# Kernel optimization log

Measured on AMD Instinct MI355X. Metric: run time of the kernel, lower is better.

Reference implementation:

```python
import jax, jax.numpy as jnp
import numpy as np
from jax import lax

NUM_L2 = 9
# hierarchical validity table: level1 pred 0 -> classes 0..3, pred 1 -> classes 4..8
_VALID = np.full((2, NUM_L2), -np.inf, dtype=np.float32)
_VALID[0, 0:4] = 0.0
_VALID[1, 4:9] = 0.0
MASK_TABLE = jnp.asarray(_VALID)


def setup_inputs() -> dict:
    key = jax.random.key(0)
    ks = jax.random.split(key, 8)
    B, C, H, W = 64, 18, 224, 224
    x = jax.random.normal(ks[0], (B, C, H, W), dtype=jnp.float32)
    model1_pred = jax.random.normal(ks[1], (B, 2), dtype=jnp.float32)
    conv_w = jax.random.normal(ks[2], (32, 18, 3, 3), dtype=jnp.float32) * 0.05
    conv_b = jax.random.normal(ks[3], (32,), dtype=jnp.float32) * 0.05
    fc1_w = jax.random.normal(ks[4], (64, 34), dtype=jnp.float32) * 0.05
    fc1_b = jax.random.normal(ks[5], (64,), dtype=jnp.float32) * 0.05
    fc2_w = jax.random.normal(ks[6], (NUM_L2, 64), dtype=jnp.float32) * 0.05
    fc2_b = jax.random.normal(ks[7], (NUM_L2,), dtype=jnp.float32) * 0.05
    return {"x": x, "model1_pred": model1_pred, "conv_w": conv_w, "conv_b": conv_b,
            "fc1_w": fc1_w, "fc1_b": fc1_b, "fc2_w": fc2_w, "fc2_b": fc2_b}


def reference(x, model1_pred, conv_w, conv_b, fc1_w, fc1_b, fc2_w, fc2_b):
    # conv 18->32, k3, pad 1 (SAME), NCHW
    h = lax.conv_general_dilated(
        x, conv_w, window_strides=(1, 1), padding='SAME',
        dimension_numbers=('NCHW', 'OIHW', 'NCHW'))
    h = jax.nn.relu(h + conv_b[None, :, None, None])
    g = h.mean(axis=(2, 3))                          # [B, 32] global average pool
    f = jnp.concatenate([g, model1_pred], axis=1)    # [B, 34]
    f = jax.nn.relu(f @ fc1_w.T + fc1_b)             # [B, 64]
    logits = f @ fc2_w.T + fc2_b                     # [B, 9]
    idx = jnp.argmax(model1_pred, axis=1)            # [B] level-1 prediction
    mask = MASK_TABLE[idx]                           # gather instead of host loop
    return jax.nn.softmax(logits + mask, axis=1)
```

## Files before the change

kernel.cpp:

```cpp
#include <hip/hip_runtime.h>
#include <math.h>

typedef _Float16 f16;
typedef _Float16 f16x2 __attribute__((ext_vector_type(2)));
typedef _Float16 f16x8 __attribute__((ext_vector_type(8)));
typedef float f32x16 __attribute__((ext_vector_type(16)));

#define BATCH 64
#define IC 18
#define OC 32
#define H 224
#define W 224
#define RSTRIP 28
#define NSTRIP 8
#define NTILE 7
#define WPB 4
#define KPW (NTILE * NSTRIP)
#define UNITS (BATCH * KPW)
#define NBLOCK (UNITS / WPB)
#define RECS 34
#define RECW 24
#define SLOTF (RECS * RECW)
#define BSTRIDE 72
#define NUM_L2 9

#define MF(a_, b_, c_) c_ = __builtin_amdgcn_mfma_f32_32x32x16_f16((a_), (b_), (c_), 0, 0, 0)

__global__ __launch_bounds__(256, 4)
void conv_mfma_kernel(const float* __restrict__ x,
                      const float* __restrict__ conv_w,
                      const float* __restrict__ conv_b,
                      float* __restrict__ part) {
    __shared__ __align__(16) f16 slab[WPB][4][SLOTF];
    __shared__ __align__(16) f16 Bw[3 * 32 * BSTRIDE];

    const int tid = threadIdx.x;
    const int l   = tid & 63;
    const int wv  = tid >> 6;
    const int lm  = l & 31;
    const int lh  = l >> 5;

    const int unit = blockIdx.x * WPB + wv;
    const int b    = unit / KPW;
    const int rem  = unit - b * KPW;
    const int t    = rem % NTILE;
    const int s    = rem / NTILE;
    const int r0   = s * RSTRIP;
    const int col0 = t * 32 - 1;

    for (int idx = tid; idx < 3 * 32 * 64; idx += 256) {
        const int kh = idx >> 11;
        const int oc = (idx >> 6) & 31;
        const int kp = idx & 63;
        int kw = 0, ic = 0, valid = 1;
        if (kp < 18)      { kw = 0; ic = kp; }
        else if (kp < 20) { kw = 2; ic = 16 + (kp - 18); }
        else if (kp < 24) { valid = 0; }
        else if (kp < 42) { kw = 1; ic = kp - 24; }
        else if (kp < 48) { valid = 0; }
        else              { kw = 2; ic = kp - 48; }
        Bw[(kh * 32 + oc) * BSTRIDE + kp] =
            (f16)(valid ? conv_w[oc * 162 + ic * 9 + kh * 3 + kw] : 0.f);
    }

    for (int i = l; i < 4 * RECS; i += 64) {
        const int sl  = i / RECS;
        const int rec = i - sl * RECS;
        f16* q = &slab[wv][sl][rec * RECW];
        f16x2 z2; z2[0] = (f16)0.f; z2[1] = (f16)0.f;
        *reinterpret_cast<f16x2*>(&q[20]) = z2;
        *reinterpret_cast<f16x2*>(&q[22]) = z2;
        if (rec >= 32) *reinterpret_cast<f16x2*>(&q[18]) = z2;
    }
    __syncthreads();

    const int p   = l >> 1;
    const int hh  = l & 1;
    const int col = col0 + p;
    const bool colok = (col >= 0) & (col < W);
    const size_t plane = (size_t)H * W;
    const float* xb = x + ((size_t)b * IC + 8 * hh) * plane + col;
    const int er   = 32 + (l >> 1);
    const int ecol = col0 + er;
    const bool eok = (l < 4) & (ecol < W);
    const float* xe = x + ((size_t)b * IC + 8 * hh) * plane + ecol;

    auto STAGE_LOAD = [&](int g, float* sv, float* sve) {
        const bool rok = (g >= 0) & (g < H);
        if (rok & colok) {
            const float* q = xb + (size_t)g * W;
            #pragma unroll
            for (int j = 0; j < 8; ++j) sv[j] = q[j * plane];
            if (hh) { sv[8] = q[8 * plane]; sv[9] = q[9 * plane]; }
            else    { sv[8] = 0.f; sv[9] = 0.f; }
        } else {
            #pragma unroll
            for (int j = 0; j < 10; ++j) sv[j] = 0.f;
        }
        if (l < 4) {
            if (rok & eok) {
                const float* q = xe + (size_t)g * W;
                #pragma unroll
                for (int j = 0; j < 8; ++j) sve[j] = q[j * plane];
                if (hh) { sve[8] = q[8 * plane]; sve[9] = q[9 * plane]; }
                else    { sve[8] = 0.f; sve[9] = 0.f; }
            } else {
                #pragma unroll
                for (int j = 0; j < 10; ++j) sve[j] = 0.f;
            }
        }
    };
    auto STAGE_WRITE = [&](int slot, const float* sv, const float* sve) {
        f16* sw = &slab[wv][slot][0];
        f16x8 v;
        #pragma unroll
        for (int j = 0; j < 8; ++j) v[j] = (f16)sv[j];
        *reinterpret_cast<f16x8*>(&sw[p * RECW + 8 * hh]) = v;
        if (hh) {
            f16x2 c2; c2[0] = (f16)sv[8]; c2[1] = (f16)sv[9];
            *reinterpret_cast<f16x2*>(&sw[p * RECW + 16]) = c2;
            if (p >= 2)
                *reinterpret_cast<f16x2*>(&sw[(p - 2) * RECW + 18]) = c2;
        }
        if (l < 4) {
            f16x8 w8;
            #pragma unroll
            for (int j = 0; j < 8; ++j) w8[j] = (f16)sve[j];
            *reinterpret_cast<f16x8*>(&sw[er * RECW + 8 * hh]) = w8;
            if (hh) {
                f16x2 e2; e2[0] = (f16)sve[8]; e2[1] = (f16)sve[9];
                *reinterpret_cast<f16x2*>(&sw[er * RECW + 16]) = e2;
                *reinterpret_cast<f16x2*>(&sw[(er - 2) * RECW + 18]) = e2;
            }
        }
    };

    for (int g = r0 - 1; g <= r0 + 1; ++g) {
        float sv[10], sve[10];
        STAGE_LOAD(g, sv, sve);
        STAGE_WRITE(g & 3, sv, sve);
    }

    f16x8 bfr[3][4];
    #pragma unroll
    for (int kh = 0; kh < 3; ++kh)
        #pragma unroll
        for (int cc = 0; cc < 4; ++cc)
            bfr[kh][cc] = *reinterpret_cast<const f16x8*>(
                &Bw[(kh * 32 + lm) * BSTRIDE + 16 * cc + 8 * lh]);

    const float bias = conv_b[lm];
    float pacc = 0.f;
    f32x16 acc;
    #pragma unroll
    for (int i = 0; i < 16; ++i) acc[i] = 0.f;

    const int abase = RECW * lm + 8 * lh;

    for (int r = r0; r < r0 + RSTRIP; ++r) {
        const bool do_stage = (r != r0 + RSTRIP - 1);
        float sv[10], sve[10];
        if (do_stage) STAGE_LOAD(r + 2, sv, sve);

        #pragma unroll
        for (int kh = 0; kh < 3; ++kh) {
            const f16* sb = &slab[wv][(r - 1 + kh) & 3][0];
            const f16x8 a0 = *reinterpret_cast<const f16x8*>(&sb[abase]);
            const f16x8 a1 = *reinterpret_cast<const f16x8*>(&sb[abase + 16]);
            const f16x8 a2 = *reinterpret_cast<const f16x8*>(&sb[abase + 32]);
            const f16x8 a3 = *reinterpret_cast<const f16x8*>(&sb[abase + 48]);
            MF(a0, bfr[kh][0], acc); MF(a1, bfr[kh][1], acc);
            MF(a2, bfr[kh][2], acc); MF(a3, bfr[kh][3], acc);
        }

        float ssum = 0.f;
        #pragma unroll
        for (int i = 0; i < 16; ++i) ssum += fmaxf(acc[i] + bias, 0.f);
        pacc += ssum;
        #pragma unroll
        for (int i = 0; i < 16; ++i) acc[i] = 0.f;

        if (do_stage) STAGE_WRITE((r + 2) & 3, sv, sve);
    }

    pacc += __shfl_xor(pacc, 32);
    if (l < 32) part[((size_t)b * KPW + rem) * 32 + lm] = pacc;
}

__global__ void head_kernel(const float* __restrict__ part,
                            const float* __restrict__ pred,
                            const float* __restrict__ fc1_w,
                            const float* __restrict__ fc1_b,
                            const float* __restrict__ fc2_w,
                            const float* __restrict__ fc2_b,
                            float* __restrict__ out) {
    __shared__ float feat[34];
    __shared__ float fsh[64];
    __shared__ float lsh[NUM_L2];
    const int b = blockIdx.x;
    const int tI = threadIdx.x;

    if (tI < 32) {
        float sres = 0.f;
        const float* pp = part + (size_t)b * KPW * 32 + tI;
        for (int k = 0; k < KPW; ++k) sres += pp[k * 32];
        feat[tI] = sres * (1.f / (float)(H * W));
    } else if (tI < 34) {
        feat[tI] = pred[b * 2 + (tI - 32)];
    }
    __syncthreads();

    {
        float sum = fc1_b[tI];
        #pragma unroll
        for (int k = 0; k < 34; ++k) sum += feat[k] * fc1_w[tI * 34 + k];
        fsh[tI] = fmaxf(sum, 0.f);
    }
    __syncthreads();

    if (tI < NUM_L2) {
        float sum = fc2_b[tI];
        #pragma unroll
        for (int j = 0; j < 64; ++j) sum += fsh[j] * fc2_w[tI * 64 + j];
        lsh[tI] = sum;
    }
    __syncthreads();

    if (tI == 0) {
        const int idx = (pred[b * 2 + 1] > pred[b * 2 + 0]) ? 1 : 0;
        const int lo = idx ? 4 : 0;
        const int hi = idx ? 9 : 4;
        float m = -1e30f;
        for (int c = lo; c < hi; ++c) m = fmaxf(m, lsh[c]);
        float e[NUM_L2];
        float ssum = 0.f;
        for (int c = 0; c < NUM_L2; ++c) {
            const float v = (c >= lo && c < hi) ? expf(lsh[c] - m) : 0.f;
            e[c] = v;
            ssum += v;
        }
        const float rs = 1.f / ssum;
        for (int c = 0; c < NUM_L2; ++c) out[b * NUM_L2 + c] = e[c] * rs;
    }
}

extern "C" void kernel_launch(void* const* d_in, const int* in_sizes, int n_in,
                              void* d_out, int out_size, void* d_ws, size_t ws_size,
                              hipStream_t stream) {
    const float* x      = (const float*)d_in[0];
    const float* pred   = (const float*)d_in[1];
    const float* conv_w = (const float*)d_in[2];
    const float* conv_b = (const float*)d_in[3];
    const float* fc1_w  = (const float*)d_in[4];
    const float* fc1_b  = (const float*)d_in[5];
    const float* fc2_w  = (const float*)d_in[6];
    const float* fc2_b  = (const float*)d_in[7];
    float* out  = (float*)d_out;
    float* part = (float*)d_ws;

    conv_mfma_kernel<<<NBLOCK, 256, 0, stream>>>(x, conv_w, conv_b, part);
    head_kernel<<<BATCH, 64, 0, stream>>>(part, pred, fc1_w, fc1_b, fc2_w, fc2_b, out);
}
```

Before: 365.9 us.

## Reuse each staged input row across three rotating output-row accumulators

The conv loop now walks input rows instead of output rows. Each LDS A-fragment is loaded once and multiplied with all three kh weight slices into three rotating accumulators, one per pending output row. This cuts LDS reads per output row by three and shrinks the per-wave slab ring from four rows to two. The cost is two extra 16-float accumulators per lane, so launch bounds drop from 4 to 3 blocks per CU, which may reduce occupancy and latency hiding.

```diff
diff --git a/kernel.cpp b/kernel.cpp
--- a/kernel.cpp
+++ b/kernel.cpp
@@ -18,6 +18,7 @@
 #define KPW (NTILE * NSTRIP)
 #define UNITS (BATCH * KPW)
 #define NBLOCK (UNITS / WPB)
+#define NITER 30
 #define RECS 34
 #define RECW 24
 #define SLOTF (RECS * RECW)
@@ -26,12 +27,12 @@
 
 #define MF(a_, b_, c_) c_ = __builtin_amdgcn_mfma_f32_32x32x16_f16((a_), (b_), (c_), 0, 0, 0)
 
-__global__ __launch_bounds__(256, 4)
+__global__ __launch_bounds__(256, 3)
 void conv_mfma_kernel(const float* __restrict__ x,
                       const float* __restrict__ conv_w,
                       const float* __restrict__ conv_b,
                       float* __restrict__ part) {
-    __shared__ __align__(16) f16 slab[WPB][4][SLOTF];
+    __shared__ __align__(16) f16 slab[WPB][2][SLOTF];
     __shared__ __align__(16) f16 Bw[3 * 32 * BSTRIDE];
 
     const int tid = threadIdx.x;
@@ -63,9 +64,9 @@
             (f16)(valid ? conv_w[oc * 162 + ic * 9 + kh * 3 + kw] : 0.f);
     }
 
-    for (int i = l; i < 4 * RECS; i += 64) {
-        const int sl  = i / RECS;
-        const int rec = i - sl * RECS;
+    for (int i = l; i < 2 * RECS; i += 64) {
+        const int sl  = (i >= RECS) ? 1 : 0;
+        const int rec = sl ? (i - RECS) : i;
         f16* q = &slab[wv][sl][rec * RECW];
         f16x2 z2; z2[0] = (f16)0.f; z2[1] = (f16)0.f;
         *reinterpret_cast<f16x2*>(&q[20]) = z2;
@@ -135,10 +136,10 @@
         }
     };
 
-    for (int g = r0 - 1; g <= r0 + 1; ++g) {
+    {
         float sv[10], sve[10];
-        STAGE_LOAD(g, sv, sve);
-        STAGE_WRITE(g & 3, sv, sve);
+        STAGE_LOAD(r0 - 1, sv, sve);
+        STAGE_WRITE(1, sv, sve);
     }
 
     f16x8 bfr[3][4];
@@ -151,36 +152,54 @@
 
     const float bias = conv_b[lm];
     float pacc = 0.f;
-    f32x16 acc;
+    f32x16 a0c, a1c, a2c;
     #pragma unroll
-    for (int i = 0; i < 16; ++i) acc[i] = 0.f;
+    for (int i = 0; i < 16; ++i) { a0c[i] = 0.f; a1c[i] = 0.f; a2c[i] = 0.f; }
 
     const int abase = RECW * lm + 8 * lh;
 
-    for (int r = r0; r < r0 + RSTRIP; ++r) {
-        const bool do_stage = (r != r0 + RSTRIP - 1);
+    auto ITER = [&](int gi, f32x16& aK0, f32x16& aK1, f32x16& aK2, int RD) {
+        const int g = r0 - 1 + gi;
+        const bool do_stage = (gi != NITER - 1);
         float sv[10], sve[10];
-        if (do_stage) STAGE_LOAD(r + 2, sv, sve);
-
-        #pragma unroll
-        for (int kh = 0; kh < 3; ++kh) {
-            const f16* sb = &slab[wv][(r - 1 + kh) & 3][0];
-            const f16x8 a0 = *reinterpret_cast<const f16x8*>(&sb[abase]);
-            const f16x8 a1 = *reinterpret_cast<const f16x8*>(&sb[abase + 16]);
-            const f16x8 a2 = *reinterpret_cast<const f16x8*>(&sb[abase + 32]);
-            const f16x8 a3 = *reinterpret_cast<const f16x8*>(&sb[abase + 48]);
-            MF(a0, bfr[kh][0], acc); MF(a1, bfr[kh][1], acc);
-            MF(a2, bfr[kh][2], acc); MF(a3, bfr[kh][3], acc);
-        }
-
+        if (do_stage) STAGE_LOAD(g + 1, sv, sve);
+
+        const f16* sb = &slab[wv][RD][0];
+        const f16x8 a0 = *reinterpret_cast<const f16x8*>(&sb[abase]);
+        const f16x8 a1 = *reinterpret_cast<const f16x8*>(&sb[abase + 16]);
+        const f16x8 a2 = *reinterpret_cast<const f16x8*>(&sb[abase + 32]);
+        const f16x8 a3 = *reinterpret_cast<const f16x8*>(&sb[abase + 48]);
+
+        if (gi >= 3) {
+            float ssum = 0.f;
+            #pragma unroll
+            for (int i = 0; i < 16; ++i) ssum += fmaxf(aK0[i] + bias, 0.f);
+            pacc += ssum;
+        }
+        #pragma unroll
+        for (int i = 0; i < 16; ++i) aK0[i] = 0.f;
+
+        MF(a0, bfr[0][0], aK0); MF(a0, bfr[1][0], aK1); MF(a0, bfr[2][0], aK2);
+        MF(a1, bfr[0][1], aK0); MF(a1, bfr[1][1], aK1); MF(a1, bfr[2][1], aK2);
+        MF(a2, bfr[0][2], aK0); MF(a2, bfr[1][2], aK1); MF(a2, bfr[2][2], aK2);
+        MF(a3, bfr[0][3], aK0); MF(a3, bfr[1][3], aK1); MF(a3, bfr[2][3], aK2);
+
+        if (do_stage) STAGE_WRITE(RD ^ 1, sv, sve);
+    };
+
+    for (int g6 = 0; g6 < NITER; g6 += 6) {
+        ITER(g6 + 0, a2c, a1c, a0c, 1);
+        ITER(g6 + 1, a0c, a2c, a1c, 0);
+        ITER(g6 + 2, a1c, a0c, a2c, 1);
+        ITER(g6 + 3, a2c, a1c, a0c, 0);
+        ITER(g6 + 4, a0c, a2c, a1c, 1);
+        ITER(g6 + 5, a1c, a0c, a2c, 0);
+    }
+    {
         float ssum = 0.f;
         #pragma unroll
-        for (int i = 0; i < 16; ++i) ssum += fmaxf(acc[i] + bias, 0.f);
+        for (int i = 0; i < 16; ++i) ssum += fmaxf(a2c[i] + bias, 0.f);
         pacc += ssum;
-        #pragma unroll
-        for (int i = 0; i < 16; ++i) acc[i] = 0.f;
-
-        if (do_stage) STAGE_WRITE((r + 2) & 3, sv, sve);
     }
 
     pacc += __shfl_xor(pacc, 32);
```

New measurement: 526.9 us. +44.0%, slower.
